# Optimization experiments

Measured on AMD Instinct MI355X. Metric: run time of the kernel, lower is better.

## Reference

```python
import jax, jax.numpy as jnp
import numpy as np

# Dynamics: f(t, y) = tanh(y @ W1 + b1) @ W2 + b2  (time-invariant MLP ode_func)
# Solver: classic fixed-grid RK4, one step per interval of time_steps_to_predict,
# matching torchdiffeq's method='rk4' on the supplied time grid.

B, X, H, T = 64, 1024, 4096, 64


def setup_inputs() -> dict:
    key = jax.random.key(0)
    k1, k2, k3 = jax.random.split(key, 3)
    x = jax.random.normal(k1, (B, 1, X), dtype=jnp.float32)
    ts = jnp.linspace(0.0, 1.0, T, dtype=jnp.float32)
    # small init so tanh-MLP dynamics stay stable over [0, 1]
    W1 = jax.random.normal(k2, (X, H), dtype=jnp.float32) * (1.0 / np.sqrt(X))
    b1 = jnp.zeros((H,), dtype=jnp.float32)
    W2 = jax.random.normal(k3, (H, X), dtype=jnp.float32) * (1.0 / np.sqrt(H))
    b2 = jnp.zeros((X,), dtype=jnp.float32)
    return {"x": x, "time_steps_to_predict": ts, "W1": W1, "b1": b1, "W2": W2, "b2": b2}


def reference(x, time_steps_to_predict, W1, b1, W2, b2):
    def f(t, y):  # y: (B, 1, X)
        del t  # time-invariant dynamics
        return jnp.tanh(y @ W1 + b1) @ W2 + b2

    ts = time_steps_to_predict

    def rk4_step(y, t_pair):
        t0, t1 = t_pair
        dt = t1 - t0
        half = dt * 0.5
        k1 = f(t0, y)
        k2 = f(t0 + half, y + half * k1)
        k3 = f(t0 + half, y + half * k2)
        k4 = f(t1, y + dt * k3)
        y_next = y + (dt / 6.0) * (k1 + 2.0 * k2 + 2.0 * k3 + k4)
        return y_next, y_next

    t_pairs = (ts[:-1], ts[1:])
    _, ys = jax.lax.scan(rk4_step, x, t_pairs)          # (T-1, B, 1, X)
    pred = jnp.concatenate([x[None], ys], axis=0)        # (T, B, 1, X)
    pred = jnp.transpose(pred, (1, 0, 2, 3))[:, :, 0, :]  # (B, T, X)
    return pred
```

## Files before the change

kernel.cpp:

```cpp
#include <hip/hip_runtime.h>
#include <hip/hip_bf16.h>
#include <cstdint>


#define NBLK 256
#define NTHR 256
#define X_   1024
#define H_   4096
#define T_   64
#define NEV  252

typedef __bf16 bf16_t;
typedef __attribute__((ext_vector_type(8))) __bf16 bf16x8;
typedef __attribute__((ext_vector_type(4))) float  f32x4;
typedef __attribute__((ext_vector_type(2))) uint32_t u32x2;
typedef __attribute__((ext_vector_type(4))) uint32_t u32x4;

#define WS_FLAGS 0
#define WS_YIN   32768
#define WS_H     (32768 + 131072)
#define WS_P     (32768 + 131072 + 524288)
#define WS_NEED  (WS_P + 786432)

__device__ inline void store_coh_b16(bf16_t* p, float v) {
  uint32_t d = (uint32_t)__builtin_bit_cast(uint16_t, (bf16_t)v);
  asm volatile("global_store_short %0, %1, off sc0 sc1" :: "v"(p), "v"(d) : "memory");
}
__device__ inline void store_coh_f32(float* p, float v) {
  asm volatile("global_store_dword %0, %1, off sc0 sc1" :: "v"(p), "v"(v) : "memory");
}
__device__ inline void store_coh_b64(bf16_t* p, u32x2 v) {
  asm volatile("global_store_dwordx2 %0, %1, off sc0 sc1" :: "v"(p), "v"(v) : "memory");
}
__device__ inline void store_coh_f32x4(float* p, f32x4 v) {
  asm volatile("global_store_dwordx4 %0, %1, off sc0 sc1" :: "v"(p), "v"(v) : "memory");
}
__device__ inline void store_flag(uint32_t* p, uint32_t v) {
  asm volatile("global_store_dword %0, %1, off sc0 sc1" :: "v"(p), "v"(v) : "memory");
}
__device__ inline uint32_t load_flag(const uint32_t* p) {
  uint32_t v;
  asm volatile("global_load_dword %0, %1, off sc0 sc1\n\ts_waitcnt vmcnt(0)"
               : "=v"(v) : "v"(p) : "memory");
  return v;
}
__device__ inline void load3_coh(const float* p0, const float* p1, const float* p2,
                                 f32x4& a, f32x4& b, f32x4& c) {
  asm volatile(
      "global_load_dwordx4 %0, %3, off sc0 sc1\n\t"
      "global_load_dwordx4 %1, %4, off sc0 sc1\n\t"
      "global_load_dwordx4 %2, %5, off sc0 sc1\n\t"
      "s_waitcnt vmcnt(0)"
      : "=&v"(a), "=&v"(b), "=&v"(c)
      : "v"(p0), "v"(p1), "v"(p2) : "memory");
}
__device__ inline uint32_t pkbf(float a, float b) {
  return (uint32_t)__builtin_bit_cast(uint16_t, (bf16_t)a)
       | ((uint32_t)__builtin_bit_cast(uint16_t, (bf16_t)b) << 16);
}

#define LDG(dst, P, OFF) \
  asm volatile("global_load_dwordx4 %0, %1, off offset:" OFF " sc0 sc1" \
               : "=v"(dst) : "v"(P))
#define DECL8(P) u32x4 P##0, P##1, P##2, P##3, P##4, P##5, P##6, P##7
#define LD8(P, PTR) \
  LDG(P##0, PTR, "0");   LDG(P##1, PTR, "64");  LDG(P##2, PTR, "128"); \
  LDG(P##3, PTR, "192"); LDG(P##4, PTR, "256"); LDG(P##5, PTR, "320"); \
  LDG(P##6, PTR, "384"); LDG(P##7, PTR, "448")
#define WAITV0 do { asm volatile("s_waitcnt vmcnt(0)" ::: "memory"); \
  __builtin_amdgcn_sched_barrier(0); } while (0)
#define BC(q) __builtin_bit_cast(bf16x8, q)

#define POLL(SLOTEXPR, NLANES, TARGET) do { \
  if (w == 0 && l < (NLANES)) { \
    uint32_t* _p = flags + (SLOTEXPR) * 16; \
    uint32_t _v = load_flag(_p); \
    while (_v < (TARGET)) { __builtin_amdgcn_s_sleep(1); _v = load_flag(_p); } \
  } \
  __syncthreads(); \
  __builtin_amdgcn_sched_barrier(0); \
} while (0)

__global__ void __launch_bounds__(NTHR, 1) node_rk4_kernel(
    const float* __restrict__ x, const float* __restrict__ ts,
    const float* __restrict__ W1, const float* __restrict__ b1,
    const float* __restrict__ W2, const float* __restrict__ b2,
    float* __restrict__ out, uint8_t* __restrict__ ws)
{
  uint32_t* flags = (uint32_t*)(ws + WS_FLAGS);
  bf16_t* yin  = (bf16_t*)(ws + WS_YIN);
  bf16_t* hbuf = (bf16_t*)(ws + WS_H);
  float*  pbuf = (float*)(ws + WS_P);

  const int tid = threadIdx.x;
  const int b   = blockIdx.x;
  const int w   = tid >> 6;
  const int l   = tid & 63;
  const int lr  = l & 15;
  const int lh  = l >> 4;
  const int g16 = b >> 2;
  const int mg  = b & 3;
  const int c   = g16 & 15;
  const int q   = g16 >> 4;

  __shared__ float red[4][4][64][4];
  __shared__ float tr[4][64][4];
  __shared__ float tsl[T_];
  if (tid < T_) tsl[tid] = ts[tid];

  bf16x8 w1f[4][8], w2f[4][8];
  #pragma unroll
  for (int ct = 0; ct < 4; ct++)
    #pragma unroll
    for (int ks = 0; ks < 8; ks++)
      #pragma unroll
      for (int j = 0; j < 8; j++) {
        w1f[ct][ks][j] = (bf16_t)W1[(size_t)(w*256 + ks*32 + lh*8 + j) * H_ + g16*64 + ct*16 + lr];
        w2f[ct][ks][j] = (bf16_t)W2[(size_t)(q*1024 + w*256 + ks*32 + lh*8 + j) * X_ + c*64 + ct*16 + lr];
      }

  const float bias1 = b1[g16*64 + w*16 + lr];
  const float bias2 = b2[c*64 + w*16 + lr];

  f32x4 y = {0.f,0.f,0.f,0.f}, yac = {0.f,0.f,0.f,0.f};
  if (q == 0) {
    #pragma unroll
    for (int r = 0; r < 4; r++) {
      const int row = mg*16 + lh*4 + r, col = c*64 + w*16 + lr;
      y[r] = x[(size_t)row * X_ + col];
      store_coh_f32(&out[(size_t)row * (T_ * X_) + col], y[r]);
      store_coh_b16(yin + (size_t)row * X_ + col, y[r]);
    }
    asm volatile("s_waitcnt vmcnt(0)" ::: "memory");
    __syncthreads();
    if (tid == 0) store_flag(flags + (256 + mg*16 + c) * 16, 1u);
  }

  for (int n = 0; n < NEV; n++) {
    const uint32_t e = (uint32_t)n + 1u;
    const int step = n >> 2, ev = n & 3;
    const float dt  = tsl[step + 1] - tsl[step];
    const float dth = 0.5f * dt, dt6 = dt * (1.f / 6.f), dt3 = dt * (1.f / 3.f);

    POLL(256 + mg*16 + l, 16, e);
    {
      bf16x8 af[8];
      {
        DECL8(qa);
        const bf16_t* ap = yin + (size_t)(mg*16 + lr) * X_ + w*256 + lh*8;
        LD8(qa, ap);
        WAITV0;
        af[0]=BC(qa0); af[1]=BC(qa1); af[2]=BC(qa2); af[3]=BC(qa3);
        af[4]=BC(qa4); af[5]=BC(qa5); af[6]=BC(qa6); af[7]=BC(qa7);
      }
      #pragma unroll
      for (int ct = 0; ct < 4; ct++) {
        f32x4 a = {0.f,0.f,0.f,0.f};
        #pragma unroll
        for (int ks = 0; ks < 8; ks++)
          a = __builtin_amdgcn_mfma_f32_16x16x32_bf16(af[ks], w1f[ct][ks], a, 0, 0, 0);
        *(f32x4*)&red[w][ct][l][0] = a;
      }
      __syncthreads();
      f32x4 h4;
      #pragma unroll
      for (int r = 0; r < 4; r++)
        h4[r] = tanhf(red[0][w][l][r] + red[1][w][l][r] + red[2][w][l][r] + red[3][w][l][r] + bias1);
      *(f32x4*)&tr[w][l][0] = h4;
      const int trow = l >> 2, tc0 = (l & 3) * 4;
      float v0 = tr[w][(trow >> 2) * 16 + tc0 + 0][trow & 3];
      float v1 = tr[w][(trow >> 2) * 16 + tc0 + 1][trow & 3];
      float v2 = tr[w][(trow >> 2) * 16 + tc0 + 2][trow & 3];
      float v3 = tr[w][(trow >> 2) * 16 + tc0 + 3][trow & 3];
      u32x2 pk; pk[0] = pkbf(v0, v1); pk[1] = pkbf(v2, v3);
      store_coh_b64(hbuf + (size_t)(mg*16 + trow) * H_ + g16*64 + w*16 + tc0, pk);
    }
    asm volatile("s_waitcnt vmcnt(0)" ::: "memory");
    __syncthreads();
    if (tid == 0) store_flag(flags + (mg*64 + g16) * 16, e);

    POLL(mg*64 + q*16 + l, 16, e);
    f32x4 p4;
    {
      bf16x8 bfr[8];
      {
        DECL8(qb);
        const bf16_t* bp = hbuf + (size_t)(mg*16 + lr) * H_ + q*1024 + w*256 + lh*8;
        LD8(qb, bp);
        WAITV0;
        bfr[0]=BC(qb0); bfr[1]=BC(qb1); bfr[2]=BC(qb2); bfr[3]=BC(qb3);
        bfr[4]=BC(qb4); bfr[5]=BC(qb5); bfr[6]=BC(qb6); bfr[7]=BC(qb7);
      }
      #pragma unroll
      for (int ct = 0; ct < 4; ct++) {
        f32x4 a = {0.f,0.f,0.f,0.f};
        #pragma unroll
        for (int ks = 0; ks < 8; ks++)
          a = __builtin_amdgcn_mfma_f32_16x16x32_bf16(bfr[ks], w2f[ct][ks], a, 0, 0, 0);
        *(f32x4*)&red[w][ct][l][0] = a;
      }
      __syncthreads();
      #pragma unroll
      for (int r = 0; r < 4; r++)
        p4[r] = red[0][w][l][r] + red[1][w][l][r] + red[2][w][l][r] + red[3][w][l][r];
    }

    if (q != 0) {
      float* ps = pbuf + ((size_t)(mg*16 + c) * 3 + (q - 1)) * 1024 + w*256 + l*4;
      store_coh_f32x4(ps, p4);
      asm volatile("s_waitcnt vmcnt(0)" ::: "memory");
      __syncthreads();
      if (tid == 0) store_flag(flags + (320 + (mg*16 + c) * 3 + (q - 1)) * 16, e);
    } else {
      POLL(320 + (mg*16 + c) * 3 + l, 3, e);
      const float* pb = pbuf + (size_t)(mg*16 + c) * 3 * 1024 + w*256 + l*4;
      f32x4 pa_, pb_, pc_;
      load3_coh(pb, pb + 1024, pb + 2048, pa_, pb_, pc_);
      #pragma unroll
      for (int r = 0; r < 4; r++) {
        const float kv = p4[r] + pa_[r] + pb_[r] + pc_[r] + bias2;
        float ypub;
        if (ev == 0)      { yac[r] = y[r] + dt6 * kv; ypub = y[r] + dth * kv; }
        else if (ev == 1) { yac[r] += dt3 * kv;       ypub = y[r] + dth * kv; }
        else if (ev == 2) { yac[r] += dt3 * kv;       ypub = y[r] + dt * kv;  }
        else              { y[r] = yac[r] + dt6 * kv; ypub = y[r]; }
        const int row = mg*16 + lh*4 + r, col = c*64 + w*16 + lr;
        store_coh_b16(yin + (size_t)row * X_ + col, ypub);
        if (ev == 3)
          store_coh_f32(&out[(size_t)row * (T_ * X_) + (size_t)(step + 1) * X_ + col], y[r]);
      }
      asm volatile("s_waitcnt vmcnt(0)" ::: "memory");
      __syncthreads();
      if (tid == 0) store_flag(flags + (256 + mg*16 + c) * 16, e + 1u);
    }
  }
}

extern "C" void kernel_launch(void* const* d_in, const int* in_sizes, int n_in,
                              void* d_out, int out_size, void* d_ws, size_t ws_size,
                              hipStream_t stream) {
  const float* x  = (const float*)d_in[0];
  const float* ts = (const float*)d_in[1];
  const float* W1 = (const float*)d_in[2];
  const float* b1 = (const float*)d_in[3];
  const float* W2 = (const float*)d_in[4];
  const float* b2 = (const float*)d_in[5];
  float* out = (float*)d_out;
  uint8_t* ws = (uint8_t*)d_ws;
  if (ws_size < (size_t)WS_NEED) return;
  hipMemsetAsync(d_ws, 0, 32768, stream);

  void* args[] = {(void*)&x, (void*)&ts, (void*)&W1, (void*)&b1,
                  (void*)&W2, (void*)&b2, (void*)&out, (void*)&ws};
  hipError_t err = hipLaunchCooperativeKernel((void*)node_rk4_kernel,
                                              dim3(NBLK), dim3(NTHR), args, 0, stream);
  if (err != hipSuccess) {
    node_rk4_kernel<<<dim3(NBLK), dim3(NTHR), 0, stream>>>(x, ts, W1, b1, W2, b2, out, ws);
  }
}
```

Baseline: 2.084 ms.

## Ring-buffer y and h exchanges so reads use cached loads with periodic invalidation

Replaces the single shared y and h exchange buffers with a 16-slot ring indexed by evaluation number. The operand loads drop the sc0 sc1 coherent bits and can hit in cache, because each slot is freshly addressed. A buffer_inv is issued every RING evaluations to drop stale lines before slots are reused. The LDS reduction layout is also transposed to [r][l] to change the bank access pattern. This trades a larger workspace and a subtle coherence argument (stale lines may survive if invalidation timing is wrong) for fewer uncached global reads on the latency-bound critical path.

Measured after the change: 2.196 ms. 5.4% more time.

```diff
diff --git a/kernel.cpp b/kernel.cpp
--- a/kernel.cpp
+++ b/kernel.cpp
@@ -9,6 +9,9 @@
 #define H_   4096
 #define T_   64
 #define NEV  252
+#define RING 16
+#define YSLOT 132096u
+#define HSLOT 525312u
 
 typedef __bf16 bf16_t;
 typedef __attribute__((ext_vector_type(8))) __bf16 bf16x8;
@@ -18,8 +21,8 @@
 
 #define WS_FLAGS 0
 #define WS_YIN   32768
-#define WS_H     (32768 + 131072)
-#define WS_P     (32768 + 131072 + 524288)
+#define WS_H     (32768 + RING * YSLOT)
+#define WS_P     (WS_H + RING * HSLOT)
 #define WS_NEED  (WS_P + 786432)
 
 __device__ inline void store_coh_b16(bf16_t* p, float v) {
@@ -59,14 +62,14 @@
        | ((uint32_t)__builtin_bit_cast(uint16_t, (bf16_t)b) << 16);
 }
 
-#define LDG(dst, P, OFF) \
-  asm volatile("global_load_dwordx4 %0, %1, off offset:" OFF " sc0 sc1" \
+#define LDGP(dst, P, OFF) \
+  asm volatile("global_load_dwordx4 %0, %1, off offset:" OFF \
                : "=v"(dst) : "v"(P))
 #define DECL8(P) u32x4 P##0, P##1, P##2, P##3, P##4, P##5, P##6, P##7
-#define LD8(P, PTR) \
-  LDG(P##0, PTR, "0");   LDG(P##1, PTR, "64");  LDG(P##2, PTR, "128"); \
-  LDG(P##3, PTR, "192"); LDG(P##4, PTR, "256"); LDG(P##5, PTR, "320"); \
-  LDG(P##6, PTR, "384"); LDG(P##7, PTR, "448")
+#define LD8P(P, PTR) \
+  LDGP(P##0, PTR, "0");   LDGP(P##1, PTR, "64");  LDGP(P##2, PTR, "128"); \
+  LDGP(P##3, PTR, "192"); LDGP(P##4, PTR, "256"); LDGP(P##5, PTR, "320"); \
+  LDGP(P##6, PTR, "384"); LDGP(P##7, PTR, "448")
 #define WAITV0 do { asm volatile("s_waitcnt vmcnt(0)" ::: "memory"); \
   __builtin_amdgcn_sched_barrier(0); } while (0)
 #define BC(q) __builtin_bit_cast(bf16x8, q)
@@ -88,9 +91,7 @@
     float* __restrict__ out, uint8_t* __restrict__ ws)
 {
   uint32_t* flags = (uint32_t*)(ws + WS_FLAGS);
-  bf16_t* yin  = (bf16_t*)(ws + WS_YIN);
-  bf16_t* hbuf = (bf16_t*)(ws + WS_H);
-  float*  pbuf = (float*)(ws + WS_P);
+  float*    pbuf  = (float*)(ws + WS_P);
 
   const int tid = threadIdx.x;
   const int b   = blockIdx.x;
@@ -103,7 +104,7 @@
   const int c   = g16 & 15;
   const int q   = g16 >> 4;
 
-  __shared__ float red[4][4][64][4];
+  __shared__ float red[4][4][4][64];
   __shared__ float tr[4][64][4];
   __shared__ float tsl[T_];
   if (tid < T_) tsl[tid] = ts[tid];
@@ -124,12 +125,13 @@
 
   f32x4 y = {0.f,0.f,0.f,0.f}, yac = {0.f,0.f,0.f,0.f};
   if (q == 0) {
+    bf16_t* yslot0 = (bf16_t*)(ws + WS_YIN);
     #pragma unroll
     for (int r = 0; r < 4; r++) {
       const int row = mg*16 + lh*4 + r, col = c*64 + w*16 + lr;
       y[r] = x[(size_t)row * X_ + col];
       store_coh_f32(&out[(size_t)row * (T_ * X_) + col], y[r]);
-      store_coh_b16(yin + (size_t)row * X_ + col, y[r]);
+      store_coh_b16(yslot0 + (size_t)row * X_ + col, y[r]);
     }
     asm volatile("s_waitcnt vmcnt(0)" ::: "memory");
     __syncthreads();
@@ -142,13 +144,21 @@
     const float dt  = tsl[step + 1] - tsl[step];
     const float dth = 0.5f * dt, dt6 = dt * (1.f / 6.f), dt3 = dt * (1.f / 3.f);
 
+    bf16_t* yin_rd = (bf16_t*)(ws + WS_YIN + (size_t)(n % RING) * YSLOT);
+    bf16_t* yin_wr = (bf16_t*)(ws + WS_YIN + (size_t)((n + 1) % RING) * YSLOT);
+    bf16_t* hbuf   = (bf16_t*)(ws + WS_H   + (size_t)(n % RING) * HSLOT);
+
     POLL(256 + mg*16 + l, 16, e);
+    if ((n & (RING - 1)) == 0) {
+      asm volatile("buffer_inv sc0 sc1\n\ts_waitcnt vmcnt(0)" ::: "memory");
+      __builtin_amdgcn_sched_barrier(0);
+    }
     {
       bf16x8 af[8];
       {
         DECL8(qa);
-        const bf16_t* ap = yin + (size_t)(mg*16 + lr) * X_ + w*256 + lh*8;
-        LD8(qa, ap);
+        const bf16_t* ap = yin_rd + (size_t)(mg*16 + lr) * X_ + w*256 + lh*8;
+        LD8P(qa, ap);
         WAITV0;
         af[0]=BC(qa0); af[1]=BC(qa1); af[2]=BC(qa2); af[3]=BC(qa3);
         af[4]=BC(qa4); af[5]=BC(qa5); af[6]=BC(qa6); af[7]=BC(qa7);
@@ -159,13 +169,14 @@
         #pragma unroll
         for (int ks = 0; ks < 8; ks++)
           a = __builtin_amdgcn_mfma_f32_16x16x32_bf16(af[ks], w1f[ct][ks], a, 0, 0, 0);
-        *(f32x4*)&red[w][ct][l][0] = a;
+        #pragma unroll
+        for (int r = 0; r < 4; r++) red[w][ct][r][l] = a[r];
       }
       __syncthreads();
       f32x4 h4;
       #pragma unroll
       for (int r = 0; r < 4; r++)
-        h4[r] = tanhf(red[0][w][l][r] + red[1][w][l][r] + red[2][w][l][r] + red[3][w][l][r] + bias1);
+        h4[r] = tanhf(red[0][w][r][l] + red[1][w][r][l] + red[2][w][r][l] + red[3][w][r][l] + bias1);
       *(f32x4*)&tr[w][l][0] = h4;
       const int trow = l >> 2, tc0 = (l & 3) * 4;
       float v0 = tr[w][(trow >> 2) * 16 + tc0 + 0][trow & 3];
@@ -186,7 +197,7 @@
       {
         DECL8(qb);
         const bf16_t* bp = hbuf + (size_t)(mg*16 + lr) * H_ + q*1024 + w*256 + lh*8;
-        LD8(qb, bp);
+        LD8P(qb, bp);
         WAITV0;
         bfr[0]=BC(qb0); bfr[1]=BC(qb1); bfr[2]=BC(qb2); bfr[3]=BC(qb3);
         bfr[4]=BC(qb4); bfr[5]=BC(qb5); bfr[6]=BC(qb6); bfr[7]=BC(qb7);
@@ -197,12 +208,13 @@
         #pragma unroll
         for (int ks = 0; ks < 8; ks++)
           a = __builtin_amdgcn_mfma_f32_16x16x32_bf16(bfr[ks], w2f[ct][ks], a, 0, 0, 0);
-        *(f32x4*)&red[w][ct][l][0] = a;
+        #pragma unroll
+        for (int r = 0; r < 4; r++) red[w][ct][r][l] = a[r];
       }
       __syncthreads();
       #pragma unroll
       for (int r = 0; r < 4; r++)
-        p4[r] = red[0][w][l][r] + red[1][w][l][r] + red[2][w][l][r] + red[3][w][l][r];
+        p4[r] = red[0][w][r][l] + red[1][w][r][l] + red[2][w][r][l] + red[3][w][r][l];
     }
 
     if (q != 0) {
@@ -225,7 +237,7 @@
         else if (ev == 2) { yac[r] += dt3 * kv;       ypub = y[r] + dt * kv;  }
         else              { y[r] = yac[r] + dt6 * kv; ypub = y[r]; }
         const int row = mg*16 + lh*4 + r, col = c*64 + w*16 + lr;
-        store_coh_b16(yin + (size_t)row * X_ + col, ypub);
+        store_coh_b16(yin_wr + (size_t)row * X_ + col, ypub);
         if (ev == 3)
           store_coh_f32(&out[(size_t)row * (T_ * X_) + (size_t)(step + 1) * X_ + col], y[r]);
       }
```
